# Optimization experiments

Measured on AMD Instinct MI355X. Metric: run time of the kernel, lower is better.

Reference implementation:

```python
import jax, jax.numpy as jnp
import numpy as np

N = 150000      # active voxels
C = 64          # head input channels
KK = 9          # 3x3 kernel offsets
H = W = 700     # BEV feature map
BN_EPS = 1e-5
HEADS = [("heatmap", 3), ("center", 2), ("center_z", 1), ("dim", 3), ("rot", 2)]


def _build_neighbor_table(seed=0):
    """Submanifold 3x3 neighbor indices for N active voxels on an HxW grid.
    Entry -1 means the neighbor site is inactive (contributes zero)."""
    rng = np.random.default_rng(seed)
    flat = rng.choice(H * W, size=N, replace=False)
    ys, xs = flat // W, flat % W
    lut = np.full(H * W, -1, np.int64)
    lut[flat] = np.arange(N)
    nbr = np.full((N, KK), -1, np.int64)
    k = 0
    for dy in (-1, 0, 1):
        for dx in (-1, 0, 1):
            ny, nx = ys + dy, xs + dx
            valid = (ny >= 0) & (ny < H) & (nx >= 0) & (nx < W)
            nf = np.where(valid, ny * W + nx, 0)
            nbr[:, k] = np.where(valid, lut[nf], -1)
            k += 1
    return nbr


def setup_inputs() -> dict:
    key = jax.random.key(0)
    ks = jax.random.split(key, 2 + 2 * len(HEADS))
    inp = {
        "features": jax.random.normal(ks[0], (N, C), jnp.float32),
        "nbr_idx": jnp.asarray(_build_neighbor_table(), jnp.int32),
        # one 3x3 subm conv per head, stacked: [n_heads, 9, C_in, C_out]
        "W3": jax.random.normal(ks[1], (len(HEADS), KK, C, C), jnp.float32) * 0.05,
        "gamma": jnp.ones((len(HEADS), C), jnp.float32),
        "beta": jnp.zeros((len(HEADS), C), jnp.float32),
    }
    for i, (name, oc) in enumerate(HEADS):
        inp[f"W1_{name}"] = jax.random.normal(ks[2 + i], (C, oc), jnp.float32) * 0.001
        if name == "heatmap":
            inp[f"b1_{name}"] = jnp.full((oc,), -float(np.log((1 - 0.01) / 0.01)), jnp.float32)
        else:
            inp[f"b1_{name}"] = jnp.zeros((oc,), jnp.float32)
    return inp


def _forward(features, nbr_idx, W3, gamma, beta, W1s, b1s):
    valid = nbr_idx >= 0                                  # [N, 9]
    idx = jnp.where(valid, nbr_idx, 0)
    # gather active-neighbor features; missing neighbors -> zero (subm conv)
    gathered = features[idx] * valid[..., None].astype(features.dtype)  # [N, 9, C]
    # all heads share the same input sparse tensor -> batched gather-GEMM
    h = jnp.einsum('nkc,hkco->hno', gathered, W3)         # [n_heads, N, C]
    # BatchNorm1d (training-mode batch stats, biased var) + ReLU
    mean = h.mean(axis=1, keepdims=True)
    var = ((h - mean) ** 2).mean(axis=1, keepdims=True)
    hn = (h - mean) * jax.lax.rsqrt(var + BN_EPS)
    hn = jax.nn.relu(hn * gamma[:, None, :] + beta[:, None, :])
    # per-head 1x1 subm conv == linear on active features
    return tuple(hn[i] @ W1s[i] + b1s[i] for i in range(len(HEADS)))


def reference(features, nbr_idx, W3, gamma, beta,
              W1_heatmap, b1_heatmap, W1_center, b1_center,
              W1_center_z, b1_center_z, W1_dim, b1_dim, W1_rot, b1_rot):
    W1s = [W1_heatmap, W1_center, W1_center_z, W1_dim, W1_rot]
    b1s = [b1_heatmap, b1_center, b1_center_z, b1_dim, b1_rot]
    return _forward(features, nbr_idx, W3, gamma, beta, W1s, b1s)
```

## Files before the change

kernel.cpp:

```cpp
#include <hip/hip_runtime.h>

#define NVOX 150000
#define BM 128
#define MTILES 1172
#define SROW 150016
#define NCOL 320

typedef __attribute__((ext_vector_type(8))) short bf16x8;
typedef __attribute__((ext_vector_type(4))) float f32x4;

__device__ __forceinline__ unsigned short f2bf(float f) {
    unsigned u = __builtin_bit_cast(unsigned, f);
    u += 0x7fffu + ((u >> 16) & 1u);
    return (unsigned short)(u >> 16);
}

__device__ __forceinline__ void gld16(const void* g, void* l) {
    __builtin_amdgcn_global_load_lds(
        (const __attribute__((address_space(1))) unsigned int*)g,
        (__attribute__((address_space(3))) unsigned int*)l, 16, 0, 0);
}

__global__ void prep_all(const float* __restrict__ src, unsigned short* __restrict__ dst,
                         const float* __restrict__ w3, unsigned short* __restrict__ bt,
                         float* __restrict__ stats) {
    int bid = blockIdx.x, tid = threadIdx.x;
    if (bid < 4688) {
        int i = bid * 256 + tid;
        if (i < NVOX * 8) {
            const float* s = src + (size_t)i * 8;
            float4 a = *(const float4*)s;
            float4 b = *(const float4*)(s + 4);
            union { bf16x8 v; unsigned short u[8]; } r;
            r.u[0] = f2bf(a.x); r.u[1] = f2bf(a.y); r.u[2] = f2bf(a.z); r.u[3] = f2bf(a.w);
            r.u[4] = f2bf(b.x); r.u[5] = f2bf(b.y); r.u[6] = f2bf(b.z); r.u[7] = f2bf(b.w);
            *(bf16x8*)(dst + (size_t)i * 8) = r.v;
        } else if (i < NVOX * 8 + 8) {
            bf16x8 z = {0, 0, 0, 0, 0, 0, 0, 0};
            *(bf16x8*)(dst + (size_t)i * 8) = z;
        }
    } else {
        int i = (bid - 4688) * 256 + tid;
        int h = i / 36864;
        int rem = i - h * 36864;
        int kk = rem >> 12;
        int c = (rem >> 6) & 63;
        int o = rem & 63;
        bt[(size_t)(((h * 9 + kk) * 8) + (c >> 3)) * 512 + o * 8 + (c & 7)] = f2bf(w3[i]);
        if (i < 2 * NCOL) stats[i] = 0.f;
    }
}

__global__ __launch_bounds__(512, 2)
void gemm_kernel(const unsigned short* __restrict__ featB,
                 const unsigned short* __restrict__ Bt2,
                 const int* __restrict__ nbr,
                 unsigned short* __restrict__ hbuf,
                 float* __restrict__ stats,
                 float* __restrict__ partials) {
    __shared__ __align__(16) char smem[93184];
    constexpr int IDX_OFF = 32768;
    constexpr int SRED_OFF = 88064;

    int mtile = blockIdx.x;
    int m0 = mtile * BM;

    int tid = threadIdx.x;
    int w = tid >> 6, lane = tid & 63;
    int quad = lane >> 4, m16 = lane & 15;

    for (int lin = tid; lin < BM * 9; lin += 512) {
        int row = lin / 9, kkq = lin - row * 9;
        int v = -1;
        if (m0 + row < NVOX) v = nbr[(size_t)(m0 + row) * 9 + kkq];
        *(int*)(smem + IDX_OFF + (kkq * BM + row) * 4) = ((v < 0) ? NVOX : v) * 128;
    }
    __syncthreads();

    f32x4 acc[4][5];
#pragma unroll
    for (int mt = 0; mt < 4; ++mt)
#pragma unroll
        for (int nt = 0; nt < 5; ++nt)
            acc[mt][nt] = (f32x4){0.f, 0.f, 0.f, 0.f};

    const char* fb = (const char*)featB;
    const char* bt = (const char*)Bt2;
    char* sAb[2] = {smem, smem + 16384};

    int mrow = (w >> 2) * 64;
    int cbase = (w & 3) * 80;

    int rloc = lane >> 3, j = lane & 7;
    int jx = (j ^ rloc) * 16;

    int bOff[5];
#pragma unroll
    for (int nt = 0; nt < 5; ++nt) {
        int c = cbase + nt * 16 + m16;
        bOff[nt] = (c >> 6) * 73728 + quad * 1024 + (c & 63) * 16;
    }
    int aRow[4];
#pragma unroll
    for (int mt = 0; mt < 4; ++mt)
        aRow[mt] = (mrow + mt * 16 + m16) * 128;
    int axor = m16 & 7;

    bf16x8 breg[2][2][5];

    auto stageA = [&](int buf, int kk) {
        char* sA = sAb[buf];
        int off0 = *(const int*)(smem + IDX_OFF + (kk * BM + w * 16 + rloc) * 4);
        int off1 = *(const int*)(smem + IDX_OFF + (kk * BM + w * 16 + 8 + rloc) * 4);
        gld16(fb + off0 + jx, sA + w * 2048);
        gld16(fb + off1 + jx, sA + w * 2048 + 1024);
    };
    auto loadB = [&](int p, int kk) {
#pragma unroll
        for (int nt = 0; nt < 5; ++nt) {
            breg[p][0][nt] = *(const bf16x8*)(bt + (size_t)(bOff[nt] + kk * 8192));
            breg[p][1][nt] = *(const bf16x8*)(bt + (size_t)(bOff[nt] + kk * 8192 + 4096));
        }
    };

    stageA(0, 0);
    loadB(0, 0);

#pragma unroll
    for (int kk = 0; kk < 9; ++kk) {
        const int p = kk & 1;
        if (kk < 8) {
            stageA(p ^ 1, kk + 1);
            loadB(p ^ 1, kk + 1);
            asm volatile("s_waitcnt vmcnt(12)" ::: "memory");
        } else {
            asm volatile("s_waitcnt vmcnt(0)" ::: "memory");
        }
        asm volatile("s_barrier" ::: "memory");
        __builtin_amdgcn_sched_barrier(0);
        __builtin_amdgcn_s_setprio(1);
#pragma unroll
        for (int ks = 0; ks < 2; ++ks) {
            bf16x8 af[4];
            int xq = ((ks * 4 + quad) ^ axor) * 16;
#pragma unroll
            for (int mt = 0; mt < 4; ++mt)
                af[mt] = *(const bf16x8*)(sAb[p] + aRow[mt] + xq);
#pragma unroll
            for (int mt = 0; mt < 4; ++mt)
#pragma unroll
                for (int nt = 0; nt < 5; ++nt)
                    acc[mt][nt] = __builtin_amdgcn_mfma_f32_16x16x32_bf16(
                        af[mt], breg[p][ks][nt], acc[mt][nt], 0, 0, 0);
        }
        __builtin_amdgcn_s_setprio(0);
        __builtin_amdgcn_sched_barrier(0);
        asm volatile("s_barrier" ::: "memory");
    }
    __builtin_amdgcn_sched_barrier(0);

#pragma unroll
    for (int mt = 0; mt < 4; ++mt) {
#pragma unroll
        for (int nt = 0; nt < 5; ++nt) {
            int col = cbase + nt * 16 + m16;
            int row = mrow + mt * 16 + quad * 4;
            f32x4 v = acc[mt][nt];
            unsigned lo = (unsigned)f2bf(v.x) | ((unsigned)f2bf(v.y) << 16);
            unsigned hi = (unsigned)f2bf(v.z) | ((unsigned)f2bf(v.w) << 16);
            uint2 pk; pk.x = lo; pk.y = hi;
            *(uint2*)(smem + col * 272 + row * 2) = pk;
        }
    }
    __syncthreads();
#pragma unroll
    for (int it = 0; it < 20; ++it) {
        int col = it * 16 + (tid >> 5);
        int l32 = tid & 31;
        uint2 v = *(const uint2*)(smem + col * 272 + l32 * 8);
        *(uint2*)(hbuf + (size_t)col * SROW + m0 + l32 * 4) = v;
    }

    float s[5], ss[5];
#pragma unroll
    for (int nt = 0; nt < 5; ++nt) {
        float a = 0.f, b = 0.f;
#pragma unroll
        for (int mt = 0; mt < 4; ++mt) {
            f32x4 v = acc[mt][nt];
            a += v.x + v.y + v.z + v.w;
            b += v.x * v.x + v.y * v.y + v.z * v.z + v.w * v.w;
        }
        s[nt] = a; ss[nt] = b;
        s[nt] += __shfl_xor(s[nt], 16); s[nt] += __shfl_xor(s[nt], 32);
        ss[nt] += __shfl_xor(ss[nt], 16); ss[nt] += __shfl_xor(ss[nt], 32);
    }
    if (quad == 0) {
#pragma unroll
        for (int nt = 0; nt < 5; ++nt) {
            float* p = (float*)(smem + SRED_OFF + (w * 80 + nt * 16 + m16) * 8);
            p[0] = s[nt]; p[1] = ss[nt];
        }
    }
    __syncthreads();
    if (tid < NCOL) {
        int c = tid;
        int qq = c / 80, lc = c - qq * 80;
        const float* p0 = (const float*)(smem + SRED_OFF + (qq * 80 + lc) * 8);
        const float* p1 = (const float*)(smem + SRED_OFF + ((qq + 4) * 80 + lc) * 8);
        float vsum = p0[0] + p1[0];
        float vss  = p0[1] + p1[1];
        if (partials) {
            float* pp = partials + (size_t)mtile * (2 * NCOL);
            pp[c] = vsum;
            pp[NCOL + c] = vss;
        } else {
            atomicAdd(&stats[c], vsum);
            atomicAdd(&stats[NCOL + c], vss);
        }
    }
}

__global__ __launch_bounds__(256)
void stats_reduce(const float* __restrict__ partials, float* __restrict__ stats) {
    __shared__ float red[256];
    int tid = threadIdx.x;
    int cl = tid & 31, sc = tid >> 5;
    int jcol = blockIdx.x * 32 + cl;
    int ybase = blockIdx.y * 147;
    int mlo = ybase + sc * 19;
    int mhi = ybase + 147; if (mhi > MTILES) mhi = MTILES;
    int mend = mlo + 19; if (mend > mhi) mend = mhi;
    float s = 0.f;
    for (int m = mlo; m < mend; ++m)
        s += partials[(size_t)m * (2 * NCOL) + jcol];
    red[tid] = s;
    __syncthreads();
    if (tid < 32) {
        float a = red[tid];
#pragma unroll
        for (int k = 1; k < 8; ++k) a += red[k * 32 + tid];
        atomicAdd(&stats[blockIdx.x * 32 + tid], a);
    }
}

__global__ __launch_bounds__(256)
void head_kernel(const unsigned short* __restrict__ hbuf,
                 const float* __restrict__ stats,
                 const float* __restrict__ gamma, const float* __restrict__ beta,
                 const float* __restrict__ W1_0, const float* __restrict__ W1_1,
                 const float* __restrict__ W1_2, const float* __restrict__ W1_3,
                 const float* __restrict__ W1_4,
                 const float* __restrict__ b1_0, const float* __restrict__ b1_1,
                 const float* __restrict__ b1_2, const float* __restrict__ b1_3,
                 const float* __restrict__ b1_4,
                 float* __restrict__ out) {
    __shared__ float sScale[64], sShift[64], sW1[192], sB1[3];
    int h = blockIdx.y;
    const float* W1; const float* b1; int oc; size_t obase;
    if (h == 0)      { W1 = W1_0; b1 = b1_0; oc = 3; obase = 0; }
    else if (h == 1) { W1 = W1_1; b1 = b1_1; oc = 2; obase = 450000; }
    else if (h == 2) { W1 = W1_2; b1 = b1_2; oc = 1; obase = 750000; }
    else if (h == 3) { W1 = W1_3; b1 = b1_3; oc = 3; obase = 900000; }
    else             { W1 = W1_4; b1 = b1_4; oc = 2; obase = 1350000; }

    int tid = threadIdx.x;
    if (tid < 64) {
        int c = h * 64 + tid;
        float mean = stats[c] * (1.f / (float)NVOX);
        float var = stats[NCOL + c] * (1.f / (float)NVOX) - mean * mean;
        float inv = rsqrtf(var + 1e-5f);
        float sc = inv * gamma[c];
        sScale[tid] = sc;
        sShift[tid] = beta[c] - mean * sc;
    }
    for (int i = tid; i < 192; i += 256) {
        int cc = i / 3, jj = i - cc * 3;
        sW1[i] = (jj < oc) ? W1[cc * oc + jj] : 0.f;
    }
    if (tid == 0) {
        sB1[0] = b1[0];
        sB1[1] = (oc >= 2) ? b1[1] : 0.f;
        sB1[2] = (oc >= 3) ? b1[2] : 0.f;
    }
    __syncthreads();

    int n = (blockIdx.x * 256 + tid) * 4;
    if (n >= NVOX) return;
    const unsigned short* hp = hbuf + (size_t)(h * 64) * SROW + n;
    float x[4][3];
#pragma unroll
    for (int rr = 0; rr < 4; ++rr) { x[rr][0] = sB1[0]; x[rr][1] = sB1[1]; x[rr][2] = sB1[2]; }
#pragma unroll 8
    for (int cc = 0; cc < 64; ++cc) {
        uint2 raw = *(const uint2*)(hp + (size_t)cc * SROW);
        float sc = sScale[cc], sh = sShift[cc];
        float w0 = sW1[cc * 3 + 0], w1 = sW1[cc * 3 + 1], w2 = sW1[cc * 3 + 2];
        float v0 = __builtin_bit_cast(float, raw.x << 16);
        float v1 = __builtin_bit_cast(float, raw.x & 0xffff0000u);
        float v2 = __builtin_bit_cast(float, raw.y << 16);
        float v3 = __builtin_bit_cast(float, raw.y & 0xffff0000u);
        v0 = fmaxf(v0 * sc + sh, 0.f); v1 = fmaxf(v1 * sc + sh, 0.f);
        v2 = fmaxf(v2 * sc + sh, 0.f); v3 = fmaxf(v3 * sc + sh, 0.f);
        x[0][0] += v0 * w0; x[0][1] += v0 * w1; x[0][2] += v0 * w2;
        x[1][0] += v1 * w0; x[1][1] += v1 * w1; x[1][2] += v1 * w2;
        x[2][0] += v2 * w0; x[2][1] += v2 * w1; x[2][2] += v2 * w2;
        x[3][0] += v3 * w0; x[3][1] += v3 * w1; x[3][2] += v3 * w2;
    }
#pragma unroll
    for (int rr = 0; rr < 4; ++rr) {
        float* op = out + obase + (size_t)(n + rr) * oc;
        op[0] = x[rr][0];
        if (oc >= 2) op[1] = x[rr][1];
        if (oc >= 3) op[2] = x[rr][2];
    }
}

extern "C" void kernel_launch(void* const* d_in, const int* in_sizes, int n_in,
                              void* d_out, int out_size, void* d_ws, size_t ws_size,
                              hipStream_t stream) {
    const float* features = (const float*)d_in[0];
    const int* nbr        = (const int*)d_in[1];
    const float* w3       = (const float*)d_in[2];
    const float* gamma    = (const float*)d_in[3];
    const float* beta     = (const float*)d_in[4];
    const float* W1_0 = (const float*)d_in[5];  const float* b1_0 = (const float*)d_in[6];
    const float* W1_1 = (const float*)d_in[7];  const float* b1_1 = (const float*)d_in[8];
    const float* W1_2 = (const float*)d_in[9];  const float* b1_2 = (const float*)d_in[10];
    const float* W1_3 = (const float*)d_in[11]; const float* b1_3 = (const float*)d_in[12];
    const float* W1_4 = (const float*)d_in[13]; const float* b1_4 = (const float*)d_in[14];
    float* out = (float*)d_out;

    char* ws = (char*)d_ws;
    unsigned short* featB = (unsigned short*)ws;
    unsigned short* Bt2   = (unsigned short*)(ws + 19200128);
    float* stats          = (float*)(ws + 19568768);
    unsigned short* hbuf  = (unsigned short*)(ws + 19571328);
    constexpr size_t PART_OFF = 19571328 + (size_t)NCOL * SROW * 2;
    float* partials = nullptr;
    if (ws_size >= PART_OFF + (size_t)MTILES * 2 * NCOL * 4)
        partials = (float*)(ws + PART_OFF);

    prep_all<<<4688 + 720, 256, 0, stream>>>(features, featB, w3, Bt2, stats);
    gemm_kernel<<<MTILES, 512, 0, stream>>>(featB, Bt2, nbr, hbuf, stats, partials);
    if (partials)
        stats_reduce<<<dim3(20, 8), 256, 0, stream>>>(partials, stats);
    head_kernel<<<dim3(147, 5), 256, 0, stream>>>(hbuf, stats, gamma, beta,
        W1_0, W1_1, W1_2, W1_3, W1_4, b1_0, b1_1, b1_2, b1_3, b1_4, out);
}
```

Measured before the change: 224.3 us.

## Double M tile to 256 rows and stage B weights through LDS

The GEMM block now covers 256 voxel rows instead of 128, so each wave computes an 8x5 grid of MFMA tiles and every B fragment is reused across twice as many rows. B weights move from per-lane register loads to async global-to-LDS copies shared by all waves and double-buffered alongside A. The epilogue writes output in two passes through the staging buffer, and the stats reduction is retuned for half as many tiles. The trade-off is much more LDS (about 153 KB) and accumulator registers, which likely drops occupancy to one block per CU, and fewer blocks for a 150k-row problem.

```diff
diff --git a/kernel.cpp b/kernel.cpp
--- a/kernel.cpp
+++ b/kernel.cpp
@@ -1,8 +1,8 @@
 #include <hip/hip_runtime.h>
 
 #define NVOX 150000
-#define BM 128
-#define MTILES 1172
+#define BM 256
+#define MTILES 586
 #define SROW 150016
 #define NCOL 320
 
@@ -58,8 +58,9 @@
                  unsigned short* __restrict__ hbuf,
                  float* __restrict__ stats,
                  float* __restrict__ partials) {
-    __shared__ __align__(16) char smem[93184];
-    constexpr int IDX_OFF = 32768;
+    __shared__ __align__(16) char smem[156672];
+    constexpr int SB_OFF = 65536;
+    constexpr int IDX_OFF = 147456;
     constexpr int SRED_OFF = 88064;
 
     int mtile = blockIdx.x;
@@ -77,81 +78,88 @@
     }
     __syncthreads();
 
-    f32x4 acc[4][5];
-#pragma unroll
-    for (int mt = 0; mt < 4; ++mt)
+    f32x4 acc[8][5];
+#pragma unroll
+    for (int mt = 0; mt < 8; ++mt)
 #pragma unroll
         for (int nt = 0; nt < 5; ++nt)
             acc[mt][nt] = (f32x4){0.f, 0.f, 0.f, 0.f};
 
     const char* fb = (const char*)featB;
     const char* bt = (const char*)Bt2;
-    char* sAb[2] = {smem, smem + 16384};
-
-    int mrow = (w >> 2) * 64;
+
+    int half = w >> 2;
+    int mrow = half * 128;
     int cbase = (w & 3) * 80;
 
     int rloc = lane >> 3, j = lane & 7;
     int jx = (j ^ rloc) * 16;
 
-    int bOff[5];
+    int bsj[5], bdj[5];
+#pragma unroll
+    for (int jj = 0; jj < 5; ++jj) {
+        int u = w * 5 + jj;
+        int h = u >> 3, c16 = u & 7;
+        bsj[jj] = (h * 72 + c16) * 1024 + lane * 16;
+        bdj[jj] = (h * 8 + c16) * 1024;
+    }
+    int sBoff[5];
 #pragma unroll
     for (int nt = 0; nt < 5; ++nt) {
         int c = cbase + nt * 16 + m16;
-        bOff[nt] = (c >> 6) * 73728 + quad * 1024 + (c & 63) * 16;
-    }
-    int aRow[4];
-#pragma unroll
-    for (int mt = 0; mt < 4; ++mt)
-        aRow[mt] = (mrow + mt * 16 + m16) * 128;
+        sBoff[nt] = (c >> 6) * 8192 + (c & 63) * 16;
+    }
     int axor = m16 & 7;
 
-    bf16x8 breg[2][2][5];
-
     auto stageA = [&](int buf, int kk) {
-        char* sA = sAb[buf];
-        int off0 = *(const int*)(smem + IDX_OFF + (kk * BM + w * 16 + rloc) * 4);
-        int off1 = *(const int*)(smem + IDX_OFF + (kk * BM + w * 16 + 8 + rloc) * 4);
-        gld16(fb + off0 + jx, sA + w * 2048);
-        gld16(fb + off1 + jx, sA + w * 2048 + 1024);
+        char* sA = smem + buf * 32768;
+#pragma unroll
+        for (int i = 0; i < 4; ++i) {
+            int off = *(const int*)(smem + IDX_OFF + (kk * BM + w * 32 + i * 8 + rloc) * 4);
+            gld16(fb + off + jx, sA + w * 4096 + i * 1024);
+        }
     };
-    auto loadB = [&](int p, int kk) {
-#pragma unroll
-        for (int nt = 0; nt < 5; ++nt) {
-            breg[p][0][nt] = *(const bf16x8*)(bt + (size_t)(bOff[nt] + kk * 8192));
-            breg[p][1][nt] = *(const bf16x8*)(bt + (size_t)(bOff[nt] + kk * 8192 + 4096));
-        }
+    auto stageB = [&](int buf, int kk) {
+        char* sB = smem + SB_OFF + buf * 40960;
+#pragma unroll
+        for (int jj = 0; jj < 5; ++jj)
+            gld16(bt + (size_t)(bsj[jj] + kk * 8192), sB + bdj[jj]);
     };
 
     stageA(0, 0);
-    loadB(0, 0);
+    stageB(0, 0);
 
 #pragma unroll
     for (int kk = 0; kk < 9; ++kk) {
         const int p = kk & 1;
         if (kk < 8) {
             stageA(p ^ 1, kk + 1);
-            loadB(p ^ 1, kk + 1);
-            asm volatile("s_waitcnt vmcnt(12)" ::: "memory");
+            stageB(p ^ 1, kk + 1);
+            asm volatile("s_waitcnt vmcnt(9)" ::: "memory");
         } else {
             asm volatile("s_waitcnt vmcnt(0)" ::: "memory");
         }
         asm volatile("s_barrier" ::: "memory");
         __builtin_amdgcn_sched_barrier(0);
         __builtin_amdgcn_s_setprio(1);
+        const char* sA = smem + p * 32768;
+        const char* sB = smem + SB_OFF + p * 40960;
 #pragma unroll
         for (int ks = 0; ks < 2; ++ks) {
-            bf16x8 af[4];
+            bf16x8 af[8], bf[5];
             int xq = ((ks * 4 + quad) ^ axor) * 16;
 #pragma unroll
-            for (int mt = 0; mt < 4; ++mt)
-                af[mt] = *(const bf16x8*)(sAb[p] + aRow[mt] + xq);
-#pragma unroll
-            for (int mt = 0; mt < 4; ++mt)
+            for (int mt = 0; mt < 8; ++mt)
+                af[mt] = *(const bf16x8*)(sA + (mrow + mt * 16 + m16) * 128 + xq);
+#pragma unroll
+            for (int nt = 0; nt < 5; ++nt)
+                bf[nt] = *(const bf16x8*)(sB + sBoff[nt] + (ks * 4 + quad) * 1024);
+#pragma unroll
+            for (int mt = 0; mt < 8; ++mt)
 #pragma unroll
                 for (int nt = 0; nt < 5; ++nt)
                     acc[mt][nt] = __builtin_amdgcn_mfma_f32_16x16x32_bf16(
-                        af[mt], breg[p][ks][nt], acc[mt][nt], 0, 0, 0);
+                        af[mt], bf[nt], acc[mt][nt], 0, 0, 0);
         }
         __builtin_amdgcn_s_setprio(0);
         __builtin_amdgcn_sched_barrier(0);
@@ -160,25 +168,31 @@
     __builtin_amdgcn_sched_barrier(0);
 
 #pragma unroll
-    for (int mt = 0; mt < 4; ++mt) {
-#pragma unroll
-        for (int nt = 0; nt < 5; ++nt) {
-            int col = cbase + nt * 16 + m16;
-            int row = mrow + mt * 16 + quad * 4;
-            f32x4 v = acc[mt][nt];
-            unsigned lo = (unsigned)f2bf(v.x) | ((unsigned)f2bf(v.y) << 16);
-            unsigned hi = (unsigned)f2bf(v.z) | ((unsigned)f2bf(v.w) << 16);
-            uint2 pk; pk.x = lo; pk.y = hi;
-            *(uint2*)(smem + col * 272 + row * 2) = pk;
-        }
-    }
-    __syncthreads();
-#pragma unroll
-    for (int it = 0; it < 20; ++it) {
-        int col = it * 16 + (tid >> 5);
-        int l32 = tid & 31;
-        uint2 v = *(const uint2*)(smem + col * 272 + l32 * 8);
-        *(uint2*)(hbuf + (size_t)col * SROW + m0 + l32 * 4) = v;
+    for (int pass = 0; pass < 2; ++pass) {
+        if (half == pass) {
+#pragma unroll
+            for (int mt = 0; mt < 8; ++mt) {
+#pragma unroll
+                for (int nt = 0; nt < 5; ++nt) {
+                    int col = cbase + nt * 16 + m16;
+                    int row = mt * 16 + quad * 4;
+                    f32x4 v = acc[mt][nt];
+                    unsigned lo = (unsigned)f2bf(v.x) | ((unsigned)f2bf(v.y) << 16);
+                    unsigned hi = (unsigned)f2bf(v.z) | ((unsigned)f2bf(v.w) << 16);
+                    uint2 pk; pk.x = lo; pk.y = hi;
+                    *(uint2*)(smem + col * 272 + row * 2) = pk;
+                }
+            }
+        }
+        __syncthreads();
+#pragma unroll
+        for (int it = 0; it < 20; ++it) {
+            int col = it * 16 + (tid >> 5);
+            int l32 = tid & 31;
+            uint2 v = *(const uint2*)(smem + col * 272 + l32 * 8);
+            *(uint2*)(hbuf + (size_t)col * SROW + m0 + pass * 128 + l32 * 4) = v;
+        }
+        __syncthreads();
     }
 
     float s[5], ss[5];
@@ -186,7 +200,7 @@
     for (int nt = 0; nt < 5; ++nt) {
         float a = 0.f, b = 0.f;
 #pragma unroll
-        for (int mt = 0; mt < 4; ++mt) {
+        for (int mt = 0; mt < 8; ++mt) {
             f32x4 v = acc[mt][nt];
             a += v.x + v.y + v.z + v.w;
             b += v.x * v.x + v.y * v.y + v.z * v.z + v.w * v.w;
@@ -227,10 +241,10 @@
     int tid = threadIdx.x;
     int cl = tid & 31, sc = tid >> 5;
     int jcol = blockIdx.x * 32 + cl;
-    int ybase = blockIdx.y * 147;
-    int mlo = ybase + sc * 19;
-    int mhi = ybase + 147; if (mhi > MTILES) mhi = MTILES;
-    int mend = mlo + 19; if (mend > mhi) mend = mhi;
+    int ybase = blockIdx.y * 74;
+    int mhi = ybase + 74; if (mhi > MTILES) mhi = MTILES;
+    int mlo = ybase + sc * 10;
+    int mend = mlo + 10; if (mend > mhi) mend = mhi;
     float s = 0.f;
     for (int m = mlo; m < mend; ++m)
         s += partials[(size_t)m * (2 * NCOL) + jcol];
```

New measurement: 210.3 us. -6.2%, faster.

## Split gather-GEMM over output-column tiles with B staged through LDS

Applied to the files above, without the earlier changes.

The gemm kernel now launches one 256-thread block per (128-row M tile, 64-column head tile), ordered so the five N tiles of a group of eight M tiles run close together. Weights are staged into LDS with global_load_lds instead of held in per-thread registers, and the accumulator shrinks from 4x5 to 4x2 tiles. This cuts register and LDS pressure so more blocks fit per CU and the grid grows roughly fivefold. The cost is that the neighbour gather of A is repeated once per column tile, multiplying feature reads, which the grouped ordering hopes will hit in L2.

```diff
diff --git a/kernel.cpp b/kernel.cpp
--- a/kernel.cpp
+++ b/kernel.cpp
@@ -51,25 +51,31 @@
     }
 }
 
-__global__ __launch_bounds__(512, 2)
+__global__ __launch_bounds__(256, 3)
 void gemm_kernel(const unsigned short* __restrict__ featB,
                  const unsigned short* __restrict__ Bt2,
                  const int* __restrict__ nbr,
                  unsigned short* __restrict__ hbuf,
                  float* __restrict__ stats,
                  float* __restrict__ partials) {
-    __shared__ __align__(16) char smem[93184];
-    constexpr int IDX_OFF = 32768;
-    constexpr int SRED_OFF = 88064;
-
-    int mtile = blockIdx.x;
+    __shared__ __align__(16) char smem[53760];
+    constexpr int SB_OFF = 32768;
+    constexpr int IDX_OFF = 49152;
+    constexpr int SRED_OFF = 32768;
+
+    int bid = blockIdx.x;
+    int r = bid & 7, q = bid >> 3;
+    int ntile = q % 5;
+    int mtile = (q / 5) * 8 + r;
+    if (mtile >= MTILES) return;
     int m0 = mtile * BM;
+    int n0 = ntile * 64;
 
     int tid = threadIdx.x;
     int w = tid >> 6, lane = tid & 63;
     int quad = lane >> 4, m16 = lane & 15;
 
-    for (int lin = tid; lin < BM * 9; lin += 512) {
+    for (int lin = tid; lin < BM * 9; lin += 256) {
         int row = lin / 9, kkq = lin - row * 9;
         int v = -1;
         if (m0 + row < NVOX) v = nbr[(size_t)(m0 + row) * 9 + kkq];
@@ -77,62 +83,50 @@
     }
     __syncthreads();
 
-    f32x4 acc[4][5];
+    f32x4 acc[4][2];
 #pragma unroll
     for (int mt = 0; mt < 4; ++mt)
 #pragma unroll
-        for (int nt = 0; nt < 5; ++nt)
+        for (int nt = 0; nt < 2; ++nt)
             acc[mt][nt] = (f32x4){0.f, 0.f, 0.f, 0.f};
 
     const char* fb = (const char*)featB;
-    const char* bt = (const char*)Bt2;
+    const char* bsrc = (const char*)Bt2 + (size_t)ntile * 73728;
     char* sAb[2] = {smem, smem + 16384};
-
-    int mrow = (w >> 2) * 64;
-    int cbase = (w & 3) * 80;
+    char* sBb[2] = {smem + SB_OFF, smem + SB_OFF + 8192};
+
+    int mrow = (w >> 1) * 64;
+    int ncol = (w & 1) * 32;
+    int c16a = w * 2, c16b = w * 2 + 1;
 
     int rloc = lane >> 3, j = lane & 7;
     int jx = (j ^ rloc) * 16;
-
-    int bOff[5];
-#pragma unroll
-    for (int nt = 0; nt < 5; ++nt) {
-        int c = cbase + nt * 16 + m16;
-        bOff[nt] = (c >> 6) * 73728 + quad * 1024 + (c & 63) * 16;
-    }
+    int axor = m16 & 7;
     int aRow[4];
 #pragma unroll
     for (int mt = 0; mt < 4; ++mt)
         aRow[mt] = (mrow + mt * 16 + m16) * 128;
-    int axor = m16 & 7;
-
-    bf16x8 breg[2][2][5];
-
-    auto stageA = [&](int buf, int kk) {
+
+    auto stage = [&](int buf, int kk) {
         char* sA = sAb[buf];
-        int off0 = *(const int*)(smem + IDX_OFF + (kk * BM + w * 16 + rloc) * 4);
-        int off1 = *(const int*)(smem + IDX_OFF + (kk * BM + w * 16 + 8 + rloc) * 4);
-        gld16(fb + off0 + jx, sA + w * 2048);
-        gld16(fb + off1 + jx, sA + w * 2048 + 1024);
+        char* sB = sBb[buf];
+#pragma unroll
+        for (int i = 0; i < 4; ++i) {
+            int off = *(const int*)(smem + IDX_OFF + (kk * BM + w * 32 + i * 8 + rloc) * 4);
+            gld16(fb + off + jx, sA + w * 4096 + i * 1024);
+        }
+        gld16(bsrc + (kk * 8 + c16a) * 1024 + lane * 16, sB + c16a * 1024);
+        gld16(bsrc + (kk * 8 + c16b) * 1024 + lane * 16, sB + c16b * 1024);
     };
-    auto loadB = [&](int p, int kk) {
-#pragma unroll
-        for (int nt = 0; nt < 5; ++nt) {
-            breg[p][0][nt] = *(const bf16x8*)(bt + (size_t)(bOff[nt] + kk * 8192));
-            breg[p][1][nt] = *(const bf16x8*)(bt + (size_t)(bOff[nt] + kk * 8192 + 4096));
-        }
-    };
-
-    stageA(0, 0);
-    loadB(0, 0);
+
+    stage(0, 0);
 
 #pragma unroll
     for (int kk = 0; kk < 9; ++kk) {
         const int p = kk & 1;
         if (kk < 8) {
-            stageA(p ^ 1, kk + 1);
-            loadB(p ^ 1, kk + 1);
-            asm volatile("s_waitcnt vmcnt(12)" ::: "memory");
+            stage(p ^ 1, kk + 1);
+            asm volatile("s_waitcnt vmcnt(6)" ::: "memory");
         } else {
             asm volatile("s_waitcnt vmcnt(0)" ::: "memory");
         }
@@ -141,17 +135,21 @@
         __builtin_amdgcn_s_setprio(1);
 #pragma unroll
         for (int ks = 0; ks < 2; ++ks) {
-            bf16x8 af[4];
+            bf16x8 af[4], bf[2];
             int xq = ((ks * 4 + quad) ^ axor) * 16;
 #pragma unroll
             for (int mt = 0; mt < 4; ++mt)
                 af[mt] = *(const bf16x8*)(sAb[p] + aRow[mt] + xq);
 #pragma unroll
+            for (int nt = 0; nt < 2; ++nt)
+                bf[nt] = *(const bf16x8*)(sBb[p] + (ks * 4 + quad) * 1024 +
+                                          (ncol + nt * 16 + m16) * 16);
+#pragma unroll
             for (int mt = 0; mt < 4; ++mt)
 #pragma unroll
-                for (int nt = 0; nt < 5; ++nt)
+                for (int nt = 0; nt < 2; ++nt)
                     acc[mt][nt] = __builtin_amdgcn_mfma_f32_16x16x32_bf16(
-                        af[mt], breg[p][ks][nt], acc[mt][nt], 0, 0, 0);
+                        af[mt], bf[nt], acc[mt][nt], 0, 0, 0);
         }
         __builtin_amdgcn_s_setprio(0);
         __builtin_amdgcn_sched_barrier(0);
@@ -162,8 +160,8 @@
 #pragma unroll
     for (int mt = 0; mt < 4; ++mt) {
 #pragma unroll
-        for (int nt = 0; nt < 5; ++nt) {
-            int col = cbase + nt * 16 + m16;
+        for (int nt = 0; nt < 2; ++nt) {
+            int col = ncol + nt * 16 + m16;
             int row = mrow + mt * 16 + quad * 4;
             f32x4 v = acc[mt][nt];
             unsigned lo = (unsigned)f2bf(v.x) | ((unsigned)f2bf(v.y) << 16);
@@ -174,16 +172,16 @@
     }
     __syncthreads();
 #pragma unroll
-    for (int it = 0; it < 20; ++it) {
-        int col = it * 16 + (tid >> 5);
+    for (int it = 0; it < 8; ++it) {
+        int col = it * 8 + (tid >> 5);
         int l32 = tid & 31;
         uint2 v = *(const uint2*)(smem + col * 272 + l32 * 8);
-        *(uint2*)(hbuf + (size_t)col * SROW + m0 + l32 * 4) = v;
-    }
-
-    float s[5], ss[5];
-#pragma unroll
-    for (int nt = 0; nt < 5; ++nt) {
+        *(uint2*)(hbuf + (size_t)(n0 + col) * SROW + m0 + l32 * 4) = v;
+    }
+
+    float s[2], ss[2];
+#pragma unroll
+    for (int nt = 0; nt < 2; ++nt) {
         float a = 0.f, b = 0.f;
 #pragma unroll
         for (int mt = 0; mt < 4; ++mt) {
@@ -197,26 +195,26 @@
     }
     if (quad == 0) {
 #pragma unroll
-        for (int nt = 0; nt < 5; ++nt) {
-            float* p = (float*)(smem + SRED_OFF + (w * 80 + nt * 16 + m16) * 8);
+        for (int nt = 0; nt < 2; ++nt) {
+            float* p = (float*)(smem + SRED_OFF + ((w * 2 + nt) * 16 + m16) * 8);
             p[0] = s[nt]; p[1] = ss[nt];
         }
     }
     __syncthreads();
-    if (tid < NCOL) {
-        int c = tid;
-        int qq = c / 80, lc = c - qq * 80;
-        const float* p0 = (const float*)(smem + SRED_OFF + (qq * 80 + lc) * 8);
-        const float* p1 = (const float*)(smem + SRED_OFF + ((qq + 4) * 80 + lc) * 8);
+    if (tid < 64) {
+        int col = tid;
+        int half = col >> 5, nt = (col >> 4) & 1, mc = col & 15;
+        const float* p0 = (const float*)(smem + SRED_OFF + ((half * 2 + nt) * 16 + mc) * 8);
+        const float* p1 = (const float*)(smem + SRED_OFF + (((2 + half) * 2 + nt) * 16 + mc) * 8);
         float vsum = p0[0] + p1[0];
         float vss  = p0[1] + p1[1];
         if (partials) {
             float* pp = partials + (size_t)mtile * (2 * NCOL);
-            pp[c] = vsum;
-            pp[NCOL + c] = vss;
+            pp[n0 + col] = vsum;
+            pp[NCOL + n0 + col] = vss;
         } else {
-            atomicAdd(&stats[c], vsum);
-            atomicAdd(&stats[NCOL + c], vss);
+            atomicAdd(&stats[n0 + col], vsum);
+            atomicAdd(&stats[NCOL + n0 + col], vss);
         }
     }
 }
@@ -342,7 +340,7 @@
         partials = (float*)(ws + PART_OFF);
 
     prep_all<<<4688 + 720, 256, 0, stream>>>(features, featB, w3, Bt2, stats);
-    gemm_kernel<<<MTILES, 512, 0, stream>>>(featB, Bt2, nbr, hbuf, stats, partials);
+    gemm_kernel<<<8 * 5 * 147, 256, 0, stream>>>(featB, Bt2, nbr, hbuf, stats, partials);
     if (partials)
         stats_reduce<<<dim3(20, 8), 256, 0, stream>>>(partials, stats);
     head_kernel<<<dim3(147, 5), 256, 0, stream>>>(hbuf, stats, gamma, beta,
```

New measurement: 210.9 us. -6.0%, faster.
